# Optimization experiments

Measured on AMD Instinct MI355X. Metric: run time of the kernel, lower is better.

The kernel has to match this reference:

```python
import jax, jax.numpy as jnp
import numpy as np

N_ATOMS = 50000
NUM_TYPES = 8
DIM_Q = 64
NUM_NEURONS = 64


def setup_inputs() -> dict:
    key = jax.random.key(0)
    k_q, k_z, k_w0, k_w1 = jax.random.split(key, 4)
    descriptors = jax.random.normal(k_q, (N_ATOMS, DIM_Q), dtype=jnp.float32)
    Z = jax.random.randint(k_z, (N_ATOMS,), 0, NUM_TYPES, dtype=jnp.int32)
    # glorot-ish scaled init for the per-type MLP weights
    W0 = jax.random.normal(k_w0, (NUM_TYPES, DIM_Q, NUM_NEURONS), dtype=jnp.float32) * np.float32(1.0 / np.sqrt(DIM_Q))
    b0 = jnp.zeros((NUM_TYPES, NUM_NEURONS), dtype=jnp.float32)
    W1 = jax.random.normal(k_w1, (NUM_TYPES, NUM_NEURONS), dtype=jnp.float32) * np.float32(1.0 / np.sqrt(NUM_NEURONS))
    b1 = jnp.zeros((), dtype=jnp.float32)
    return {"descriptors": descriptors, "W0": W0, "b0": b0, "W1": W1, "b1": b1, "Z": Z}


def reference(descriptors, W0, b0, W1, b1, Z):
    # Per-type gather of expert weights (the headroom hotspot):
    W0_t = W0[Z]          # [N, dim_q, num_neurons]
    b0_t = b0[Z]          # [N, num_neurons]
    W1_t = W1[Z]          # [N, num_neurons]
    # Batched 1-hidden-layer MLP per atom: h_i = tanh(q_i @ W0[Z_i] + b0[Z_i])
    h = jnp.tanh(jnp.einsum('nd,ndk->nk', descriptors, W0_t) + b0_t)  # [N, num_neurons]
    # Per-atom scalar energy, global bias b1, then total energy (target_mode == 0)
    E_i = jnp.sum(h * W1_t, axis=1) + b1  # [N]
    return jnp.sum(E_i)
```

## Files before the change

kernel.cpp:

```cpp
#include <hip/hip_runtime.h>
#include <math.h>

#define NUM_TYPES 8
#define DIM 64
#define SEG 8192
#define BM 128
#define QS_STRIDE 132

__global__ __launch_bounds__(256) void scatter_kernel(
    const int* __restrict__ Z, int* __restrict__ fill, int* __restrict__ sorted,
    const float* __restrict__ b1, float* __restrict__ out, int N)
{
    __shared__ int cnt[NUM_TYPES];
    __shared__ int base[NUM_TYPES];
    int tid = threadIdx.x;
    if (tid < NUM_TYPES) cnt[tid] = 0;
    __syncthreads();

    int i = blockIdx.x * 256 + tid;
    int z = 0, r = 0;
    bool valid = (i < N);
    if (valid) {
        z = Z[i];
        r = atomicAdd(&cnt[z], 1);
    }
    __syncthreads();
    if (tid < NUM_TYPES) base[tid] = atomicAdd(&fill[tid], cnt[tid]);
    __syncthreads();
    if (valid) {
        int p = base[z] + r;
        if (p < SEG) sorted[z * SEG + p] = i;
    }
    if (i == 0) out[0] = (float)N * b1[0];
}

__global__ __launch_bounds__(256) void mlp_kernel(
    const float* __restrict__ desc, const float* __restrict__ W0,
    const float* __restrict__ b0, const float* __restrict__ W1,
    const int* __restrict__ sorted, float* __restrict__ out)
{
    __shared__ float Qs[DIM][QS_STRIDE];
    __shared__ float Ws[DIM][DIM];
    __shared__ int   slots[BM];
    __shared__ float b0s[DIM];
    __shared__ float W1s[DIM];
    __shared__ float wsum[4];

    const int t    = blockIdx.x >> 6;
    const int tile = blockIdx.x & 63;
    const int tid  = threadIdx.x;

    if (tid < BM) slots[tid] = sorted[t * SEG + tile * BM + tid];
    __syncthreads();
    if (slots[0] < 0) return;

    {
        const float4* w0v = (const float4*)(W0 + t * DIM * DIM);
        float4* wsv = (float4*)&Ws[0][0];
        #pragma unroll
        for (int i = 0; i < 4; ++i) wsv[tid + i * 256] = w0v[tid + i * 256];
        if (tid < DIM) { b0s[tid] = b0[t * DIM + tid]; W1s[tid] = W1[t * DIM + tid]; }
    }

    #pragma unroll
    for (int it = 0; it < 8; ++it) {
        int f  = tid + it * 256;
        int a  = f >> 4;
        int dv = (f & 15) << 2;
        int idx = slots[a];
        float4 q = (idx >= 0) ? *(const float4*)(desc + (size_t)idx * DIM + dv)
                              : make_float4(0.f, 0.f, 0.f, 0.f);
        Qs[dv + 0][a] = q.x; Qs[dv + 1][a] = q.y;
        Qs[dv + 2][a] = q.z; Qs[dv + 3][a] = q.w;
    }
    __syncthreads();

    const int ag = tid & 15;
    const int kg = tid >> 4;
    const int a0 = ag * 8;
    const int k0 = kg * 4;

    float acc[8][4] = {};
    #pragma unroll 4
    for (int d = 0; d < DIM; ++d) {
        float4 qa = *(const float4*)&Qs[d][a0];
        float4 qb = *(const float4*)&Qs[d][a0 + 4];
        float4 w  = *(const float4*)&Ws[d][k0];
        float q[8] = {qa.x, qa.y, qa.z, qa.w, qb.x, qb.y, qb.z, qb.w};
        #pragma unroll
        for (int i = 0; i < 8; ++i) {
            acc[i][0] += q[i] * w.x;
            acc[i][1] += q[i] * w.y;
            acc[i][2] += q[i] * w.z;
            acc[i][3] += q[i] * w.w;
        }
    }

    float bk[4], wk[4];
    #pragma unroll
    for (int j = 0; j < 4; ++j) { bk[j] = b0s[k0 + j]; wk[j] = W1s[k0 + j]; }

    float e = 0.f;
    #pragma unroll
    for (int i = 0; i < 8; ++i) {
        if (slots[a0 + i] >= 0) {
            float s = 0.f;
            #pragma unroll
            for (int j = 0; j < 4; ++j)
                s += tanhf(acc[i][j] + bk[j]) * wk[j];
            e += s;
        }
    }

    #pragma unroll
    for (int o = 32; o > 0; o >>= 1) e += __shfl_down(e, o, 64);
    if ((tid & 63) == 0) wsum[tid >> 6] = e;
    __syncthreads();
    if (tid == 0) atomicAdd(out, wsum[0] + wsum[1] + wsum[2] + wsum[3]);
}

extern "C" void kernel_launch(void* const* d_in, const int* in_sizes, int n_in,
                              void* d_out, int out_size, void* d_ws, size_t ws_size,
                              hipStream_t stream)
{
    const float* desc = (const float*)d_in[0];
    const float* W0   = (const float*)d_in[1];
    const float* b0   = (const float*)d_in[2];
    const float* W1   = (const float*)d_in[3];
    const float* b1   = (const float*)d_in[4];
    const int*   Z    = (const int*)d_in[5];
    const int N = in_sizes[5];

    int* fill   = (int*)d_ws;
    int* sorted = (int*)((char*)d_ws + 64);

    hipMemsetAsync(fill, 0, NUM_TYPES * sizeof(int), stream);
    hipMemsetAsync(sorted, 0xFF, NUM_TYPES * SEG * sizeof(int), stream);

    scatter_kernel<<<(N + 255) / 256, 256, 0, stream>>>(
        Z, fill, sorted, b1, (float*)d_out, N);

    mlp_kernel<<<NUM_TYPES * (SEG / BM), 256, 0, stream>>>(
        desc, W0, b0, W1, sorted, (float*)d_out);
}
```

Measured before the change: 91.59 us.

## Compute per-atom MLP in registers with uniform weight loads instead of LDS tiles

Each thread now owns one atom and keeps all 64 hidden activations in registers. Descriptor rows are streamed directly from global memory, and W0 rows are read as wave-uniform loads, so the shared-memory staging, transpose and barrier are gone. Tiles grow to 256 atoms per block, and tanhf is replaced with an exp-based fast approximation. The cost is heavy register pressure (64 accumulators), uncoalesced per-thread row reads of desc, and a slight loss of accuracy in tanh.

```diff
diff --git a/kernel.cpp b/kernel.cpp
--- a/kernel.cpp
+++ b/kernel.cpp
@@ -4,8 +4,7 @@
 #define NUM_TYPES 8
 #define DIM 64
 #define SEG 8192
-#define BM 128
-#define QS_STRIDE 132
+#define BA 256
 
 __global__ __launch_bounds__(256) void scatter_kernel(
     const int* __restrict__ Z, int* __restrict__ fill, int* __restrict__ sorted,
@@ -34,86 +33,62 @@
     if (i == 0) out[0] = (float)N * b1[0];
 }
 
-__global__ __launch_bounds__(256) void mlp_kernel(
+__global__ __launch_bounds__(256, 1) void mlp_kernel(
     const float* __restrict__ desc, const float* __restrict__ W0,
     const float* __restrict__ b0, const float* __restrict__ W1,
     const int* __restrict__ sorted, float* __restrict__ out)
 {
-    __shared__ float Qs[DIM][QS_STRIDE];
-    __shared__ float Ws[DIM][DIM];
-    __shared__ int   slots[BM];
-    __shared__ float b0s[DIM];
-    __shared__ float W1s[DIM];
-    __shared__ float wsum[4];
+    const int t    = blockIdx.x >> 5;
+    const int tile = blockIdx.x & 31;
+    const int tid  = threadIdx.x;
+    const int base = t * SEG + tile * BA;
 
-    const int t    = blockIdx.x >> 6;
-    const int tile = blockIdx.x & 63;
-    const int tid  = threadIdx.x;
+    if (sorted[base] < 0) return;
 
-    if (tid < BM) slots[tid] = sorted[t * SEG + tile * BM + tid];
-    __syncthreads();
-    if (slots[0] < 0) return;
+    const int  slot  = sorted[base + tid];
+    const bool valid = (slot >= 0);
+    const float4* qp = (const float4*)(desc + (size_t)(valid ? slot : 0) * DIM);
+    const float*  wp = W0 + t * (DIM * DIM);
 
-    {
-        const float4* w0v = (const float4*)(W0 + t * DIM * DIM);
-        float4* wsv = (float4*)&Ws[0][0];
+    float h[DIM];
+    #pragma unroll
+    for (int k = 0; k < DIM; ++k) h[k] = 0.f;
+
+    float4 q0 = qp[0];
+    float4 q1 = qp[1];
+
+    #pragma unroll 1
+    for (int dv = 0; dv < 16; ++dv) {
+        float4 cur = q0;
+        q0 = q1;
+        if (dv < 14) q1 = qp[dv + 2];
+        float qa[4] = {cur.x, cur.y, cur.z, cur.w};
         #pragma unroll
-        for (int i = 0; i < 4; ++i) wsv[tid + i * 256] = w0v[tid + i * 256];
-        if (tid < DIM) { b0s[tid] = b0[t * DIM + tid]; W1s[tid] = W1[t * DIM + tid]; }
-    }
-
-    #pragma unroll
-    for (int it = 0; it < 8; ++it) {
-        int f  = tid + it * 256;
-        int a  = f >> 4;
-        int dv = (f & 15) << 2;
-        int idx = slots[a];
-        float4 q = (idx >= 0) ? *(const float4*)(desc + (size_t)idx * DIM + dv)
-                              : make_float4(0.f, 0.f, 0.f, 0.f);
-        Qs[dv + 0][a] = q.x; Qs[dv + 1][a] = q.y;
-        Qs[dv + 2][a] = q.z; Qs[dv + 3][a] = q.w;
-    }
-    __syncthreads();
-
-    const int ag = tid & 15;
-    const int kg = tid >> 4;
-    const int a0 = ag * 8;
-    const int k0 = kg * 4;
-
-    float acc[8][4] = {};
-    #pragma unroll 4
-    for (int d = 0; d < DIM; ++d) {
-        float4 qa = *(const float4*)&Qs[d][a0];
-        float4 qb = *(const float4*)&Qs[d][a0 + 4];
-        float4 w  = *(const float4*)&Ws[d][k0];
-        float q[8] = {qa.x, qa.y, qa.z, qa.w, qb.x, qb.y, qb.z, qb.w};
-        #pragma unroll
-        for (int i = 0; i < 8; ++i) {
-            acc[i][0] += q[i] * w.x;
-            acc[i][1] += q[i] * w.y;
-            acc[i][2] += q[i] * w.z;
-            acc[i][3] += q[i] * w.w;
+        for (int j = 0; j < 4; ++j) {
+            const float* wr = wp + (dv * 4 + j) * DIM;
+            const float qj = qa[j];
+            #pragma unroll
+            for (int k = 0; k < DIM; ++k)
+                h[k] = fmaf(qj, wr[k], h[k]);
         }
     }
 
-    float bk[4], wk[4];
-    #pragma unroll
-    for (int j = 0; j < 4; ++j) { bk[j] = b0s[k0 + j]; wk[j] = W1s[k0 + j]; }
-
     float e = 0.f;
-    #pragma unroll
-    for (int i = 0; i < 8; ++i) {
-        if (slots[a0 + i] >= 0) {
-            float s = 0.f;
-            #pragma unroll
-            for (int j = 0; j < 4; ++j)
-                s += tanhf(acc[i][j] + bk[j]) * wk[j];
-            e += s;
+    if (valid) {
+        const float* b0r = b0 + t * DIM;
+        const float* w1r = W1 + t * DIM;
+        #pragma unroll
+        for (int k = 0; k < DIM; ++k) {
+            float x  = h[k] + b0r[k];
+            float u  = __expf(2.0f * x);
+            float th = 1.0f - __fdividef(2.0f, u + 1.0f);
+            e = fmaf(th, w1r[k], e);
         }
     }
 
     #pragma unroll
     for (int o = 32; o > 0; o >>= 1) e += __shfl_down(e, o, 64);
+    __shared__ float wsum[4];
     if ((tid & 63) == 0) wsum[tid >> 6] = e;
     __syncthreads();
     if (tid == 0) atomicAdd(out, wsum[0] + wsum[1] + wsum[2] + wsum[3]);
@@ -140,6 +115,6 @@
     scatter_kernel<<<(N + 255) / 256, 256, 0, stream>>>(
         Z, fill, sorted, b1, (float*)d_out, N);
 
-    mlp_kernel<<<NUM_TYPES * (SEG / BM), 256, 0, stream>>>(
+    mlp_kernel<<<NUM_TYPES * (SEG / BA), 256, 0, stream>>>(
         desc, W0, b0, W1, sorted, (float*)d_out);
 }
```

New measurement: 104.1 us. 13.7% more time.
